# Kernel optimization log

Hardware: AMD Instinct MI355X
Metric: run time of the kernel (lower is better)

The kernel has to match this reference:

```python
import jax, jax.numpy as jnp
import numpy as np

LN_EPS = 1e-5  # torch nn.LayerNorm default


def setup_inputs() -> dict:
    key = jax.random.key(0)
    kx, kw = jax.random.split(key)
    T, B, D = 1024, 8, 2048
    x = jax.random.normal(kx, (T, B, D), dtype=jnp.float32)
    c0 = jnp.zeros((B, D), dtype=jnp.float32)
    # Linear(n_embd, 3*n_embd, bias=False) weight: [3D, D], scaled for sane activations
    W = jax.random.normal(kw, (3 * D, D), dtype=jnp.float32) / np.sqrt(D)
    gamma = jnp.ones((D,), dtype=jnp.float32)
    beta = jnp.zeros((D,), dtype=jnp.float32)
    return {"x": x, "c0": c0, "W": W, "gamma": gamma, "beta": beta}


def reference(x, c0, W, gamma, beta):
    # x: [T, B, D], c0: [B, D], W: [3D, D]
    T, B, D = x.shape
    # Projection for all timesteps at once (same math as per-step Linear).
    ufr = jnp.einsum('tbd,ed->tbe', x, W)  # [T, B, 3D]
    u, f, r = jnp.split(ufr, 3, axis=-1)
    f = jax.nn.sigmoid(f)
    r = jax.nn.sigmoid(r)

    def step(c_prev, inp):
        x_t, u_t, f_t, r_t = inp
        c_t = f_t * c_prev + (1.0 - f_t) * u_t
        h_t = r_t * jnp.tanh(c_t) + (1.0 - r_t) * x_t
        return c_t, h_t

    c_T, h = jax.lax.scan(step, c0, (x, u, f, r))  # h: [T, B, D]

    g = jax.nn.gelu(h, approximate=False)  # torch F.gelu default = exact erf
    mean = jnp.mean(g, axis=-1, keepdims=True)
    var = jnp.var(g, axis=-1, keepdims=True)
    out = (g - mean) * jax.lax.rsqrt(var + LN_EPS) * gamma + beta
    return out, c_T
```

## Files before the change

### kernel.cpp

```cpp
#include <hip/hip_runtime.h>
#include <hip/hip_bf16.h>

#define T_DIM 1024
#define B_DIM 8
#define D_DIM 2048
#define E_DIM 6144
#define N_ROWS 8192
#define K_DIM 2048
#define LN_EPS 1e-5f

#define S2  128
#define CH2 8
#define BD (B_DIM * D_DIM)

typedef short bf16x8 __attribute__((ext_vector_type(8)));
typedef float f32x4 __attribute__((ext_vector_type(4)));

__device__ __forceinline__ unsigned short f2bf(float f) {
  unsigned u = __float_as_uint(f);
  u += 0x7fffu + ((u >> 16) & 1u);
  return (unsigned short)(u >> 16);
}
__device__ __forceinline__ float bf2f(unsigned short h) {
  return __uint_as_float(((unsigned)h) << 16);
}
__device__ __forceinline__ float fast_sigmoid(float x) {
  return __builtin_amdgcn_rcpf(1.f + __expf(-x));
}
__device__ __forceinline__ float fast_tanh(float x) {
  return 1.f - 2.f * __builtin_amdgcn_rcpf(__expf(2.f * x) + 1.f);
}

__global__ __launch_bounds__(256) void cvt_kernel(const float* __restrict__ src,
                                                  unsigned short* __restrict__ dst,
                                                  int n4) {
  int i = blockIdx.x * 256 + threadIdx.x;
  if (i < n4) {
    float4 v = reinterpret_cast<const float4*>(src)[i];
    ushort4 o;
    o.x = f2bf(v.x); o.y = f2bf(v.y); o.z = f2bf(v.z); o.w = f2bf(v.w);
    reinterpret_cast<ushort4*>(dst)[i] = o;
  }
}

#define NT2 32

__global__ __launch_bounds__(512, 2) void gemm8_kernel(
    const unsigned short* __restrict__ A,
    const unsigned short* __restrict__ Bw,
    unsigned short* __restrict__ C) {
  extern __shared__ __align__(16) char smem[];
  const int tid  = threadIdx.x;
  const int lane = tid & 63;
  const int wave = tid >> 6;
  const int wm = wave >> 2;
  const int wn = wave & 3;

  const int bid = blockIdx.x;
  const int tileM = ((bid & 7) * 4 + ((bid >> 3) & 3)) * 256;
  const int tileN = (bid >> 5) * 256;

  const int p0i = wave * 2048 + lane * 16;
  const int p1i = p0i + 1024;
  const int q0i = p0i ^ (((p0i >> 9) & 1) << 5);
  const int q1i = p1i ^ (((p1i >> 9) & 1) << 5);
  const int go0 = ((q0i >> 6) & 127) * 4096 + ((q0i >> 13) << 6) + (q0i & 63);
  const int go1 = ((q1i >> 6) & 127) * 4096 + ((q1i >> 13) << 6) + (q1i & 63);
  const char* Ab = (const char*)A + (size_t)tileM * 4096;
  const char* Bb = (const char*)Bw + (size_t)tileN * 4096;

#define STAGE(kt, h, bufOff)                                                 \
  {                                                                          \
    const char* gs_ = ((h) < 2 ? Ab : Bb) +                                  \
                      (size_t)(((h) & 1) * 128) * 4096 + (size_t)(kt) * 128; \
    char* ds_ = smem + (bufOff) + (h) * 16384 + wave * 2048;                 \
    __builtin_amdgcn_global_load_lds(                                        \
        (const __attribute__((address_space(1))) void*)(gs_ + go0),          \
        (__attribute__((address_space(3))) void*)ds_, 16, 0, 0);             \
    __builtin_amdgcn_global_load_lds(                                        \
        (const __attribute__((address_space(1))) void*)(gs_ + go1),          \
        (__attribute__((address_space(3))) void*)(ds_ + 1024), 16, 0, 0);    \
  }

  const int xbit = ((lane >> 3) & 1) << 5;
  const int aBase = wm * 16384 +
                    (((lane & 15) * 64 + (lane >> 4) * 16) ^ xbit);
  const int bBase = 32768 + (wn >> 1) * 16384 +
                    ((((wn & 1) * 64 + (lane & 15)) * 64 + (lane >> 4) * 16) ^ xbit);

#define RDA(m, bufOff)                                                          \
  a[m][0] = *reinterpret_cast<const bf16x8*>(smem + (bufOff) + aBase + (m) * 1024);        \
  a[m][1] = *reinterpret_cast<const bf16x8*>(smem + (bufOff) + aBase + (m) * 1024 + 8192);
#define RDB(n, bufOff)                                                          \
  b[n][0] = *reinterpret_cast<const bf16x8*>(smem + (bufOff) + bBase + (n) * 1024);        \
  b[n][1] = *reinterpret_cast<const bf16x8*>(smem + (bufOff) + bBase + (n) * 1024 + 8192);
#define MM(m, n)                                                                \
  acc[m][n] = __builtin_amdgcn_mfma_f32_16x16x32_bf16(a[m][0], b[n][0], acc[m][n], 0, 0, 0); \
  acc[m][n] = __builtin_amdgcn_mfma_f32_16x16x32_bf16(a[m][1], b[n][1], acc[m][n], 0, 0, 0);

  bf16x8 a[8][2], b[4][2];
  f32x4 acc[8][4] = {};

  STAGE(0, 0, 0); STAGE(0, 1, 0); STAGE(0, 2, 0); STAGE(0, 3, 0);
  STAGE(1, 0, 65536); STAGE(1, 1, 65536);
  asm volatile("s_waitcnt vmcnt(4)" ::: "memory");
  __builtin_amdgcn_s_barrier();

  for (int j = 0; j < NT2; ++j) {
    const int buf  = (j & 1) << 16;
    const int nbuf = buf ^ 65536;
    RDA(0, buf); RDA(1, buf); RDA(2, buf); RDA(3, buf);
    RDB(0, buf); RDB(1, buf);
    if (j < NT2 - 1) STAGE(j + 1, 2, nbuf);
    __builtin_amdgcn_s_barrier();
    asm volatile("s_waitcnt lgkmcnt(0)" ::: "memory");
    __builtin_amdgcn_s_setprio(1);
    MM(0, 0); MM(0, 1); MM(1, 0); MM(1, 1);
    MM(2, 0); MM(2, 1); MM(3, 0); MM(3, 1);
    __builtin_amdgcn_s_setprio(0);
    __builtin_amdgcn_s_barrier();
    RDA(4, buf); RDA(5, buf); RDA(6, buf); RDA(7, buf);
    if (j < NT2 - 1) STAGE(j + 1, 3, nbuf);
    __builtin_amdgcn_s_barrier();
    asm volatile("s_waitcnt lgkmcnt(0)" ::: "memory");
    __builtin_amdgcn_s_setprio(1);
    MM(4, 0); MM(4, 1); MM(5, 0); MM(5, 1);
    MM(6, 0); MM(6, 1); MM(7, 0); MM(7, 1);
    __builtin_amdgcn_s_setprio(0);
    __builtin_amdgcn_s_barrier();
    RDB(2, buf); RDB(3, buf);
    if (j < NT2 - 2) STAGE(j + 2, 0, buf);
    __builtin_amdgcn_s_barrier();
    asm volatile("s_waitcnt lgkmcnt(0)" ::: "memory");
    __builtin_amdgcn_s_setprio(1);
    MM(4, 2); MM(4, 3); MM(5, 2); MM(5, 3);
    MM(6, 2); MM(6, 3); MM(7, 2); MM(7, 3);
    __builtin_amdgcn_s_setprio(0);
    __builtin_amdgcn_s_barrier();
    if (j < NT2 - 2) {
      STAGE(j + 2, 1, buf);
      asm volatile("s_waitcnt vmcnt(4)" ::: "memory");
    } else if (j == NT2 - 2) {
      asm volatile("s_waitcnt vmcnt(0)" ::: "memory");
    }
    __builtin_amdgcn_s_barrier();
    __builtin_amdgcn_s_setprio(1);
    MM(0, 2); MM(0, 3); MM(1, 2); MM(1, 3);
    MM(2, 2); MM(2, 3); MM(3, 2); MM(3, 3);
    __builtin_amdgcn_s_setprio(0);
    __builtin_amdgcn_s_barrier();
  }

  const int crow = (lane >> 4) * 4;
  const int ccol = lane & 15;
#pragma unroll
  for (int m = 0; m < 8; ++m) {
#pragma unroll
    for (int n = 0; n < 4; ++n) {
#pragma unroll
      for (int jj = 0; jj < 4; ++jj) {
        int row = tileM + wm * 128 + m * 16 + crow + jj;
        int col = tileN + wn * 64 + n * 16 + ccol;
        C[(size_t)row * E_DIM + col] = f2bf(acc[m][n][jj]);
      }
    }
  }
#undef STAGE
#undef RDA
#undef RDB
#undef MM
}

__global__ __launch_bounds__(256) void scan_p1_kernel(
    const unsigned short* __restrict__ ufr,
    float* __restrict__ Aout, float* __restrict__ Bout) {
  const int idx = blockIdx.x * 256 + threadIdx.x;
  const int s = blockIdx.y;
  const int b = idx >> 11;
  const int d = idx & 2047;
  const unsigned short* up =
      ufr + ((size_t)(s * CH2) * B_DIM + b) * E_DIM + d;
  float Aacc = 1.f, Bacc = 0.f;
#pragma unroll
  for (int it = 0; it < CH2; ++it) {
    float u  = bf2f(up[0]);
    float fl = bf2f(up[D_DIM]);
    float f = fast_sigmoid(fl);
    Aacc *= f;
    Bacc = f * Bacc + (1.f - f) * u;
    up += (size_t)B_DIM * E_DIM;
  }
  Aout[(size_t)s * BD + idx] = Aacc;
  Bout[(size_t)s * BD + idx] = Bacc;
}

__global__ __launch_bounds__(256) void scan_p2_kernel(
    const float* __restrict__ c0,
    const float* __restrict__ Ain, const float* __restrict__ Bin,
    float* __restrict__ cs, float* __restrict__ cT) {
  const int idx = blockIdx.x * 256 + threadIdx.x;
  float c = c0[idx];
  for (int s = 0; s < S2; ++s) {
    cs[(size_t)s * BD + idx] = c;
    c = Ain[(size_t)s * BD + idx] * c + Bin[(size_t)s * BD + idx];
  }
  cT[idx] = c;
}

__global__ __launch_bounds__(256) void scan_p3ln_kernel(
    const float* __restrict__ x,
    const unsigned short* __restrict__ ufr,
    const float* __restrict__ cs,
    const float* __restrict__ gamma,
    const float* __restrict__ beta,
    float* __restrict__ out) {
  const int b = blockIdx.x & (B_DIM - 1);
  const int s = blockIdx.x >> 3;
  const int tid = threadIdx.x;
  const int lane = tid & 63;
  const int wave = tid >> 6;
  const int d0 = tid * 8;
  __shared__ float red[8];

  float c[8];
  {
    const float* csp = cs + (size_t)s * BD + b * D_DIM + d0;
    float4 v0 = *(const float4*)csp;
    float4 v1 = *(const float4*)(csp + 4);
    c[0]=v0.x; c[1]=v0.y; c[2]=v0.z; c[3]=v0.w;
    c[4]=v1.x; c[5]=v1.y; c[6]=v1.z; c[7]=v1.w;
  }
  float gam[8], bet[8];
  {
    float4 g0 = *(const float4*)(gamma + d0);
    float4 g1 = *(const float4*)(gamma + d0 + 4);
    float4 b0 = *(const float4*)(beta + d0);
    float4 b1 = *(const float4*)(beta + d0 + 4);
    gam[0]=g0.x; gam[1]=g0.y; gam[2]=g0.z; gam[3]=g0.w;
    gam[4]=g1.x; gam[5]=g1.y; gam[6]=g1.z; gam[7]=g1.w;
    bet[0]=b0.x; bet[1]=b0.y; bet[2]=b0.z; bet[3]=b0.w;
    bet[4]=b1.x; bet[5]=b1.y; bet[6]=b1.z; bet[7]=b1.w;
  }

  for (int it = 0; it < CH2; ++it) {
    const size_t rowo = (size_t)(s * CH2 + it) * B_DIM + b;
    const unsigned short* up = ufr + rowo * E_DIM + d0;
    const float* xp = x + rowo * D_DIM + d0;
    ushort4 uv0 = *(const ushort4*)up;
    ushort4 uv1 = *(const ushort4*)(up + 4);
    ushort4 fv0 = *(const ushort4*)(up + D_DIM);
    ushort4 fv1 = *(const ushort4*)(up + D_DIM + 4);
    ushort4 rv0 = *(const ushort4*)(up + 2 * D_DIM);
    ushort4 rv1 = *(const ushort4*)(up + 2 * D_DIM + 4);
    float4 xv0 = *(const float4*)xp;
    float4 xv1 = *(const float4*)(xp + 4);
    unsigned short uu[8] = {uv0.x, uv0.y, uv0.z, uv0.w, uv1.x, uv1.y, uv1.z, uv1.w};
    unsigned short ff[8] = {fv0.x, fv0.y, fv0.z, fv0.w, fv1.x, fv1.y, fv1.z, fv1.w};
    unsigned short rr[8] = {rv0.x, rv0.y, rv0.z, rv0.w, rv1.x, rv1.y, rv1.z, rv1.w};
    float xx[8] = {xv0.x, xv0.y, xv0.z, xv0.w, xv1.x, xv1.y, xv1.z, xv1.w};

    float g[8];
    float s1 = 0.f, sq = 0.f;
#pragma unroll
    for (int jj = 0; jj < 8; ++jj) {
      float f = fast_sigmoid(bf2f(ff[jj]));
      float r = fast_sigmoid(bf2f(rr[jj]));
      c[jj] = f * c[jj] + (1.f - f) * bf2f(uu[jj]);
      float h = r * fast_tanh(c[jj]) + (1.f - r) * xx[jj];
      float gg = 0.5f * h * (1.f + erff(h * 0.70710678118654752f));
      g[jj] = gg;
      s1 += gg;
      sq += gg * gg;
    }
#pragma unroll
    for (int off = 32; off; off >>= 1) {
      s1 += __shfl_xor(s1, off);
      sq += __shfl_xor(sq, off);
    }
    if (lane == 0) { red[wave] = s1; red[4 + wave] = sq; }
    __syncthreads();
    float S1 = red[0] + red[1] + red[2] + red[3];
    float Sq = red[4] + red[5] + red[6] + red[7];
    __syncthreads();
    float mean = S1 * (1.f / D_DIM);
    float var  = Sq * (1.f / D_DIM) - mean * mean;
    float inv = rsqrtf(var + LN_EPS);

    float* op = out + rowo * D_DIM + d0;
    float4 o0 = {(g[0] - mean) * inv * gam[0] + bet[0],
                 (g[1] - mean) * inv * gam[1] + bet[1],
                 (g[2] - mean) * inv * gam[2] + bet[2],
                 (g[3] - mean) * inv * gam[3] + bet[3]};
    float4 o1 = {(g[4] - mean) * inv * gam[4] + bet[4],
                 (g[5] - mean) * inv * gam[5] + bet[5],
                 (g[6] - mean) * inv * gam[6] + bet[6],
                 (g[7] - mean) * inv * gam[7] + bet[7]};
    *(float4*)op = o0;
    *(float4*)(op + 4) = o1;
  }
}

extern "C" void kernel_launch(void* const* d_in, const int* in_sizes, int n_in,
                              void* d_out, int out_size, void* d_ws, size_t ws_size,
                              hipStream_t stream) {
  const float* x     = (const float*)d_in[0];
  const float* c0    = (const float*)d_in[1];
  const float* W     = (const float*)d_in[2];
  const float* gamma = (const float*)d_in[3];
  const float* beta  = (const float*)d_in[4];
  float* out = (float*)d_out;
  float* cT  = out + (size_t)N_ROWS * D_DIM;

  unsigned short* ufr = (unsigned short*)d_ws;
  unsigned short* xb  = ufr + (size_t)N_ROWS * E_DIM;
  unsigned short* wb  = xb + (size_t)N_ROWS * K_DIM;

  float* Abuf = (float*)xb;
  float* Bbuf = Abuf + (size_t)S2 * BD;
  float* csb  = Bbuf + (size_t)S2 * BD;

  int nx4 = N_ROWS * K_DIM / 4;
  int nw4 = E_DIM * K_DIM / 4;
  cvt_kernel<<<(nx4 + 255) / 256, 256, 0, stream>>>(x, xb, nx4);
  cvt_kernel<<<(nw4 + 255) / 256, 256, 0, stream>>>(W, wb, nw4);

  (void)hipFuncSetAttribute((const void*)gemm8_kernel,
                            hipFuncAttributeMaxDynamicSharedMemorySize, 131072);
  gemm8_kernel<<<768, 512, 131072, stream>>>(xb, wb, ufr);

  dim3 sg(BD / 256, S2);
  scan_p1_kernel<<<sg, 256, 0, stream>>>(ufr, Abuf, Bbuf);
  scan_p2_kernel<<<BD / 256, 256, 0, stream>>>(c0, Abuf, Bbuf, csb, cT);
  scan_p3ln_kernel<<<B_DIM * S2, 256, 0, stream>>>(x, ufr, csb, gamma, beta, out);
}
```

Baseline: 277.5 us.

## Make GEMM persistent-style: each block computes three N tiles sequentially

The GEMM grid shrinks from 768 to 256 blocks, and each block loops over three N tiles, 96 k-steps in total. It keeps the double-buffered pipeline running across tile boundaries and writes out then clears the accumulators after every 32 k-steps. The aim is to avoid partial-wave tail effects from 768 blocks on 256 CUs with 2 blocks per CU, and to overlap the next tile's loads with the current epilogue. The risk is that only 256 blocks run at once, about one per CU at two-per-CU occupancy, which may reduce latency hiding.

New measurement: 282.3 us. Within noise of the previous version (+1.7%).

```diff
diff --git a/kernel.cpp b/kernel.cpp
--- a/kernel.cpp
+++ b/kernel.cpp
@@ -43,7 +43,8 @@
   }
 }
 
-#define NT2 32
+#define KT2 32
+#define NTOT 96
 
 __global__ __launch_bounds__(512, 2) void gemm8_kernel(
     const unsigned short* __restrict__ A,
@@ -56,9 +57,12 @@
   const int wm = wave >> 2;
   const int wn = wave & 3;
 
-  const int bid = blockIdx.x;
-  const int tileM = ((bid & 7) * 4 + ((bid >> 3) & 3)) * 256;
-  const int tileN = (bid >> 5) * 256;
+  const int bid   = blockIdx.x;
+  const int xcd   = bid & 7;
+  const int slot  = bid >> 3;
+  const int mgrp  = slot & 3;
+  const int nbase = slot >> 2;
+  const int tileM = (xcd * 4 + mgrp) * 256;
 
   const int p0i = wave * 2048 + lane * 16;
   const int p1i = p0i + 1024;
@@ -66,13 +70,25 @@
   const int q1i = p1i ^ (((p1i >> 9) & 1) << 5);
   const int go0 = ((q0i >> 6) & 127) * 4096 + ((q0i >> 13) << 6) + (q0i & 63);
   const int go1 = ((q1i >> 6) & 127) * 4096 + ((q1i >> 13) << 6) + (q1i & 63);
-  const char* Ab = (const char*)A + (size_t)tileM * 4096;
-  const char* Bb = (const char*)Bw + (size_t)tileN * 4096;
-
-#define STAGE(kt, h, bufOff)                                                 \
+  const char* Ab  = (const char*)A + (size_t)tileM * 4096;
+  const char* Bb0 = (const char*)Bw + (size_t)(nbase * 256) * 4096;
+  const size_t BSTRIDE = (size_t)8 * 256 * 4096;
+
+#define STAGE_A(kt, h, bufOff)                                               \
   {                                                                          \
-    const char* gs_ = ((h) < 2 ? Ab : Bb) +                                  \
-                      (size_t)(((h) & 1) * 128) * 4096 + (size_t)(kt) * 128; \
+    const char* gs_ = Ab + (size_t)((h) * 128) * 4096 + (size_t)(kt) * 128;  \
+    char* ds_ = smem + (bufOff) + (h) * 16384 + wave * 2048;                 \
+    __builtin_amdgcn_global_load_lds(                                        \
+        (const __attribute__((address_space(1))) void*)(gs_ + go0),          \
+        (__attribute__((address_space(3))) void*)ds_, 16, 0, 0);             \
+    __builtin_amdgcn_global_load_lds(                                        \
+        (const __attribute__((address_space(1))) void*)(gs_ + go1),          \
+        (__attribute__((address_space(3))) void*)(ds_ + 1024), 16, 0, 0);    \
+  }
+#define STAGE_B(kt, h, bufOff, Bbase)                                        \
+  {                                                                          \
+    const char* gs_ = (Bbase) + (size_t)(((h) & 1) * 128) * 4096 +           \
+                      (size_t)(kt) * 128;                                    \
     char* ds_ = smem + (bufOff) + (h) * 16384 + wave * 2048;                 \
     __builtin_amdgcn_global_load_lds(                                        \
         (const __attribute__((address_space(1))) void*)(gs_ + go0),          \
@@ -101,17 +117,21 @@
   bf16x8 a[8][2], b[4][2];
   f32x4 acc[8][4] = {};
 
-  STAGE(0, 0, 0); STAGE(0, 1, 0); STAGE(0, 2, 0); STAGE(0, 3, 0);
-  STAGE(1, 0, 65536); STAGE(1, 1, 65536);
+  STAGE_A(0, 0, 0); STAGE_A(0, 1, 0);
+  STAGE_B(0, 2, 0, Bb0); STAGE_B(0, 3, 0, Bb0);
+  STAGE_A(1, 0, 65536); STAGE_A(1, 1, 65536);
   asm volatile("s_waitcnt vmcnt(4)" ::: "memory");
   __builtin_amdgcn_s_barrier();
 
-  for (int j = 0; j < NT2; ++j) {
-    const int buf  = (j & 1) << 16;
+  for (int i = 0; i < NTOT; ++i) {
+    const int buf  = (i & 1) << 16;
     const int nbuf = buf ^ 65536;
+    const int i1 = i + 1, i2 = i + 2;
+    const int kt1 = i1 & 31, kt2 = i2 & 31;
+    const char* Bb1 = Bb0 + (size_t)(i1 >> 5) * BSTRIDE;
     RDA(0, buf); RDA(1, buf); RDA(2, buf); RDA(3, buf);
     RDB(0, buf); RDB(1, buf);
-    if (j < NT2 - 1) STAGE(j + 1, 2, nbuf);
+    if (i1 < NTOT) STAGE_B(kt1, 2, nbuf, Bb1);
     __builtin_amdgcn_s_barrier();
     asm volatile("s_waitcnt lgkmcnt(0)" ::: "memory");
     __builtin_amdgcn_s_setprio(1);
@@ -120,7 +140,7 @@
     __builtin_amdgcn_s_setprio(0);
     __builtin_amdgcn_s_barrier();
     RDA(4, buf); RDA(5, buf); RDA(6, buf); RDA(7, buf);
-    if (j < NT2 - 1) STAGE(j + 1, 3, nbuf);
+    if (i1 < NTOT) STAGE_B(kt1, 3, nbuf, Bb1);
     __builtin_amdgcn_s_barrier();
     asm volatile("s_waitcnt lgkmcnt(0)" ::: "memory");
     __builtin_amdgcn_s_setprio(1);
@@ -129,7 +149,7 @@
     __builtin_amdgcn_s_setprio(0);
     __builtin_amdgcn_s_barrier();
     RDB(2, buf); RDB(3, buf);
-    if (j < NT2 - 2) STAGE(j + 2, 0, buf);
+    if (i2 < NTOT) STAGE_A(kt2, 0, buf);
     __builtin_amdgcn_s_barrier();
     asm volatile("s_waitcnt lgkmcnt(0)" ::: "memory");
     __builtin_amdgcn_s_setprio(1);
@@ -137,10 +157,10 @@
     MM(6, 2); MM(6, 3); MM(7, 2); MM(7, 3);
     __builtin_amdgcn_s_setprio(0);
     __builtin_amdgcn_s_barrier();
-    if (j < NT2 - 2) {
-      STAGE(j + 2, 1, buf);
+    if (i2 < NTOT) {
+      STAGE_A(kt2, 1, buf);
       asm volatile("s_waitcnt vmcnt(4)" ::: "memory");
-    } else if (j == NT2 - 2) {
+    } else if (i2 == NTOT) {
       asm volatile("s_waitcnt vmcnt(0)" ::: "memory");
     }
     __builtin_amdgcn_s_barrier();
@@ -149,23 +169,27 @@
     MM(2, 2); MM(2, 3); MM(3, 2); MM(3, 3);
     __builtin_amdgcn_s_setprio(0);
     __builtin_amdgcn_s_barrier();
-  }
-
-  const int crow = (lane >> 4) * 4;
-  const int ccol = lane & 15;
-#pragma unroll
-  for (int m = 0; m < 8; ++m) {
-#pragma unroll
-    for (int n = 0; n < 4; ++n) {
-#pragma unroll
-      for (int jj = 0; jj < 4; ++jj) {
-        int row = tileM + wm * 128 + m * 16 + crow + jj;
-        int col = tileN + wn * 64 + n * 16 + ccol;
-        C[(size_t)row * E_DIM + col] = f2bf(acc[m][n][jj]);
+    if ((i & 31) == 31) {
+      const int tileN = (nbase + 8 * (i >> 5)) * 256;
+      const int crow = (lane >> 4) * 4;
+      const int ccol = lane & 15;
+#pragma unroll
+      for (int m = 0; m < 8; ++m) {
+#pragma unroll
+        for (int n = 0; n < 4; ++n) {
+#pragma unroll
+          for (int jj = 0; jj < 4; ++jj) {
+            int row = tileM + wm * 128 + m * 16 + crow + jj;
+            int col = tileN + wn * 64 + n * 16 + ccol;
+            C[(size_t)row * E_DIM + col] = f2bf(acc[m][n][jj]);
+          }
+          acc[m][n] = (f32x4){0.f, 0.f, 0.f, 0.f};
+        }
       }
     }
   }
-#undef STAGE
+#undef STAGE_A
+#undef STAGE_B
 #undef RDA
 #undef RDB
 #undef MM
@@ -326,7 +350,7 @@
 
   (void)hipFuncSetAttribute((const void*)gemm8_kernel,
                             hipFuncAttributeMaxDynamicSharedMemorySize, 131072);
-  gemm8_kernel<<<768, 512, 131072, stream>>>(xb, wb, ufr);
+  gemm8_kernel<<<256, 512, 131072, stream>>>(xb, wb, ufr);
 
   dim3 sg(BD / 256, S2);
   scan_p1_kernel<<<sg, 256, 0, stream>>>(ufr, Abuf, Bbuf);
```
